# Optimization experiments

Measured on AMD Instinct MI355X. Metric: run time of the kernel, lower is better.

The kernel has to match this reference:

```python
import jax, jax.numpy as jnp
import numpy as np

NUM_NODES = 65536      # 16 graphs x 4096 nodes
NODES_PER_GRAPH = 4096
NUM_GRAPHS = 16
NUM_EDGES = 1048576    # avg degree 16
DIM = 64


def setup_inputs() -> dict:
    key = jax.random.key(0)
    ks = jax.random.split(key, 10)
    # edges constrained within each component graph (batched-graph semantics)
    eper = NUM_EDGES // NUM_GRAPHS
    gid = np.repeat(np.arange(NUM_GRAPHS), eper)
    rng = np.random.default_rng(0)
    src = jnp.asarray(rng.integers(0, NODES_PER_GRAPH, NUM_EDGES) + gid * NODES_PER_GRAPH, dtype=jnp.int64)
    dst = jnp.asarray(rng.integers(0, NODES_PER_GRAPH, NUM_EDGES) + gid * NODES_PER_GRAPH, dtype=jnp.int64)
    s = 1.0 / np.sqrt(DIM)
    return {
        "x": jax.random.normal(ks[0], (NUM_NODES, DIM), dtype=jnp.float32),
        "W1": jax.random.normal(ks[1], (DIM, DIM), dtype=jnp.float32) * s,
        "b1": jnp.zeros((DIM,), dtype=jnp.float32),
        "W2": jax.random.normal(ks[2], (DIM, DIM), dtype=jnp.float32) * s,
        "b2": jnp.zeros((DIM,), dtype=jnp.float32),
        "W3": jax.random.normal(ks[3], (DIM, DIM), dtype=jnp.float32) * s,
        "b3": jnp.zeros((DIM,), dtype=jnp.float32),
        "src": src,
        "dst": dst,
        "num_graphs": NUM_GRAPHS,
    }


def _sym_norms(src, dst, n):
    ones = jnp.ones(src.shape[0], dtype=jnp.float32)
    deg_out = jax.ops.segment_sum(ones, src, num_segments=n)
    deg_in = jax.ops.segment_sum(ones, dst, num_segments=n)
    inv_sqrt = lambda d: jnp.where(d > 0, d, 1.0) ** -0.5 * (d > 0)
    return inv_sqrt(deg_out), inv_sqrt(deg_in)


def _graph_conv(x, W, b, src, dst, norm_src, norm_dst, n):
    # DGL GraphConv, norm='both': h = D_in^{-1/2} A D_out^{-1/2} (X W) + b
    h = (x * norm_src[:, None]) @ W          # [N, D]
    msg = h[src]                              # [E, D] gather
    agg = jax.ops.segment_sum(msg, dst, num_segments=n)  # [N, D] scatter-add
    return agg * norm_dst[:, None] + b


def reference(x, W1, b1, W2, b2, W3, b3, src, dst, num_graphs):
    n = x.shape[0]
    norm_src, norm_dst = _sym_norms(src, dst, n)
    h = _graph_conv(x, W1, b1, src, dst, norm_src, norm_dst, n)
    h = _graph_conv(h, W2, b2, src, dst, norm_src, norm_dst, n)
    h = _graph_conv(h, W3, b3, src, dst, norm_src, norm_dst, n)
    # unbatch + pad to max_num_nodes + stack; equal-size graphs -> pure reshape
    return h.reshape(num_graphs, n // num_graphs, h.shape[-1])
```

## Files before the change

### kernel.cpp

```cpp
#include <hip/hip_runtime.h>
#include <hip/hip_fp16.h>

#define DIM 64
#define NG  16
#define CPG 16
#define NPG 4096
#define LSTR 68
#define HISTB (NG*CPG)
#define GGN 32

__global__ __launch_bounds__(256) void k1_hist_gemm(
    const int* __restrict__ src, const int* __restrict__ dst,
    int* __restrict__ hsub, int* __restrict__ dsub, int chunk, int npg,
    const float* __restrict__ x, const float* __restrict__ W1,
    float* __restrict__ hout, int swiz)
{
    __shared__ int smem[8192];
    const int tid = threadIdx.x;
    if ((int)blockIdx.x < HISTB) {
        int* hs = smem;
        int* hd = smem + NPG;
        const int blk = blockIdx.x;
        const int g = blk / CPG;
        const int ebase = blk * chunk;
        const int nbase = g * npg;
        for (int i = tid; i < npg; i += 256) { hs[i] = 0; hd[i] = 0; }
        __syncthreads();
        for (int e = tid; e < chunk; e += 256) {
            atomicAdd(&hs[src[ebase + e] - nbase], 1);
            atomicAdd(&hd[dst[ebase + e] - nbase], 1);
        }
        __syncthreads();
        for (int i = tid; i < npg; i += 256) {
            hsub[blk * npg + i] = hs[i];
            dsub[blk * npg + i] = hd[i];
        }
    } else {
        float* Wt = (float*)smem;
        float* xs = Wt + 64 * LSTR;
        int blk = blockIdx.x - HISTB;
        if (swiz) {
            int xg = blk & 7;
            int j = blk >> 3;
            int g = xg + ((j >> 7) << 3);
            blk = (g << 7) + (j & 127);
        }
        const int row0 = blk * 32;
        for (int i = tid; i < 64 * 64; i += 256) {
            int k = i >> 6, c = i & 63;
            Wt[c * LSTR + k] = W1[i];
        }
        for (int i = tid; i < 32 * 64; i += 256) {
            int r = i >> 6, c = i & 63;
            xs[r * LSTR + c] = x[(size_t)(row0 + r) * 64 + c];
        }
        __syncthreads();
        const int c0 = tid & 31;
        const int r0 = tid >> 5;
        float acc[4][2] = {};
#pragma unroll
        for (int k = 0; k < 64; k += 4) {
            float4 w0 = *(const float4*)&Wt[(c0     ) * LSTR + k];
            float4 w1 = *(const float4*)&Wt[(c0 + 32) * LSTR + k];
#pragma unroll
            for (int rr = 0; rr < 4; ++rr) {
                float4 xv = *(const float4*)&xs[(r0 + 8 * rr) * LSTR + k];
                acc[rr][0] += xv.x * w0.x + xv.y * w0.y + xv.z * w0.z + xv.w * w0.w;
                acc[rr][1] += xv.x * w1.x + xv.y * w1.y + xv.z * w1.z + xv.w * w1.w;
            }
        }
#pragma unroll
        for (int rr = 0; rr < 4; ++rr) {
            int row = row0 + r0 + 8 * rr;
            hout[(size_t)row * 64 + c0     ] = acc[rr][0];
            hout[(size_t)row * 64 + c0 + 32] = acc[rr][1];
        }
    }
}

__global__ __launch_bounds__(1024) void k2_scan(
    const int* __restrict__ hsub, int* __restrict__ dsub,
    float* __restrict__ ns, float* __restrict__ nd,
    int* __restrict__ rowptr, int epg, int npg, int N, int E)
{
    __shared__ int ddeg[NPG];
    __shared__ int wsum[16];
    const int g = blockIdx.x;
    const int t = threadIdx.x;
    const int nbase = g * npg;
    const int ebase = g * epg;
    for (int i = t; i < npg; i += 1024) {
        int sd = 0, dd = 0;
#pragma unroll
        for (int k = 0; k < CPG; ++k) {
            sd += hsub[(g * CPG + k) * npg + i];
            dd += dsub[(g * CPG + k) * npg + i];
        }
        ns[nbase + i] = sd > 0 ? rsqrtf((float)sd) : 0.0f;
        nd[nbase + i] = dd > 0 ? rsqrtf((float)dd) : 0.0f;
        ddeg[i] = dd;
    }
    __syncthreads();
    const int i0 = 4 * t;
    int d0 = ddeg[i0], d1 = ddeg[i0 + 1], d2 = ddeg[i0 + 2], d3 = ddeg[i0 + 3];
    int s4 = d0 + d1 + d2 + d3;
    const int lane = t & 63, wid = t >> 6;
    int v = s4;
#pragma unroll
    for (int off = 1; off < 64; off <<= 1) {
        int u = __shfl_up(v, off, 64);
        if (lane >= off) v += u;
    }
    if (lane == 63) wsum[wid] = v;
    __syncthreads();
    if (t < 16) {
        int w = wsum[t];
#pragma unroll
        for (int off = 1; off < 16; off <<= 1) {
            int u = __shfl_up(w, off, 16);
            if (t >= off) w += u;
        }
        wsum[t] = w;
    }
    __syncthreads();
    int incl = v + (wid > 0 ? wsum[wid - 1] : 0);
    int c = ebase + incl - s4;
    rowptr[nbase + i0    ] = c; ddeg[i0    ] = c; c += d0;
    rowptr[nbase + i0 + 1] = c; ddeg[i0 + 1] = c; c += d1;
    rowptr[nbase + i0 + 2] = c; ddeg[i0 + 2] = c; c += d2;
    rowptr[nbase + i0 + 3] = c; ddeg[i0 + 3] = c;
    if (g == 0 && t == 0) rowptr[N] = E;
    __syncthreads();
    for (int i = t; i < npg; i += 1024) {
        int cc = ddeg[i];
#pragma unroll
        for (int k = 0; k < CPG; ++k) {
            int* p = &dsub[(g * CPG + k) * npg + i];
            int old = *p; *p = cc; cc += old;
        }
    }
}

__global__ __launch_bounds__(256) void k3_fill(
    const int* __restrict__ src, const int* __restrict__ dst,
    const int* __restrict__ dsub, int* __restrict__ ssrc, int chunk, int npg,
    const float* __restrict__ hA32, const float* __restrict__ ns,
    __half* __restrict__ hF)
{
    const int t = threadIdx.x;
    if ((int)blockIdx.x < HISTB) {
        __shared__ int cur[NPG];
        const int blk = blockIdx.x;
        const int g = blk / CPG;
        const int ebase = blk * chunk;
        const int nbase = g * npg;
        for (int i = t; i < npg; i += 256) cur[i] = dsub[blk * npg + i];
        __syncthreads();
        for (int e = t; e < chunk; e += 256) {
            int s = src[ebase + e];
            int d = dst[ebase + e] - nbase;
            int pos = atomicAdd(&cur[d], 1);
            ssrc[pos] = s;
        }
    } else {
        const int sb = blockIdx.x - HISTB;
        const int base = sb * 16384;
#pragma unroll
        for (int it = 0; it < 16; ++it) {
            int pos = base + it * 1024 + t * 4;
            float4 v = *(const float4*)(hA32 + pos);
            float s = ns[pos >> 6];
            __half2 p0 = __floats2half2_rn(v.x * s, v.y * s);
            __half2 p1 = __floats2half2_rn(v.z * s, v.w * s);
            uint2 o;
            o.x = *(const unsigned int*)&p0;
            o.y = *(const unsigned int*)&p1;
            *(uint2*)(hF + pos) = o;
        }
    }
}

__device__ __forceinline__ void acc_h4(float4& acc, uint2 u)
{
    __half2 p = *(__half2*)&u.x;
    __half2 q = *(__half2*)&u.y;
    float2 f0 = __half22float2(p);
    float2 f1 = __half22float2(q);
    acc.x += f0.x; acc.y += f0.y; acc.z += f1.x; acc.w += f1.y;
}

__device__ __forceinline__ void acc_h4s(float4& acc, uint2 u, float s)
{
    __half2 p = *(__half2*)&u.x;
    __half2 q = *(__half2*)&u.y;
    float2 f0 = __half22float2(p);
    float2 f1 = __half22float2(q);
    acc.x += s * f0.x; acc.y += s * f0.y; acc.z += s * f1.x; acc.w += s * f1.y;
}

__device__ __forceinline__ float4 gather_node(
    const __half* __restrict__ h, const int* __restrict__ ssrc,
    int beg, int end, int sub)
{
    const size_t off = (size_t)sub * 4;
    float4 acc = {0.f, 0.f, 0.f, 0.f};
    int j = beg;
    const int last = end - 8;
    if (j <= last) {
        int s0 = ssrc[j+0], s1 = ssrc[j+1], s2 = ssrc[j+2], s3 = ssrc[j+3];
        int s4 = ssrc[j+4], s5 = ssrc[j+5], s6 = ssrc[j+6], s7 = ssrc[j+7];
        uint2 a0 = *(const uint2*)(h + (size_t)s0 * 64 + off);
        uint2 a1 = *(const uint2*)(h + (size_t)s1 * 64 + off);
        uint2 a2 = *(const uint2*)(h + (size_t)s2 * 64 + off);
        uint2 a3 = *(const uint2*)(h + (size_t)s3 * 64 + off);
        uint2 a4 = *(const uint2*)(h + (size_t)s4 * 64 + off);
        uint2 a5 = *(const uint2*)(h + (size_t)s5 * 64 + off);
        uint2 a6 = *(const uint2*)(h + (size_t)s6 * 64 + off);
        uint2 a7 = *(const uint2*)(h + (size_t)s7 * 64 + off);
        j += 8;
        bool more = (j <= last);
        if (more) {
            s0 = ssrc[j+0]; s1 = ssrc[j+1]; s2 = ssrc[j+2]; s3 = ssrc[j+3];
            s4 = ssrc[j+4]; s5 = ssrc[j+5]; s6 = ssrc[j+6]; s7 = ssrc[j+7];
        }
        while (more) {
            uint2 b0 = *(const uint2*)(h + (size_t)s0 * 64 + off);
            uint2 b1 = *(const uint2*)(h + (size_t)s1 * 64 + off);
            uint2 b2 = *(const uint2*)(h + (size_t)s2 * 64 + off);
            uint2 b3 = *(const uint2*)(h + (size_t)s3 * 64 + off);
            uint2 b4 = *(const uint2*)(h + (size_t)s4 * 64 + off);
            uint2 b5 = *(const uint2*)(h + (size_t)s5 * 64 + off);
            uint2 b6 = *(const uint2*)(h + (size_t)s6 * 64 + off);
            uint2 b7 = *(const uint2*)(h + (size_t)s7 * 64 + off);
            j += 8;
            more = (j <= last);
            if (more) {
                s0 = ssrc[j+0]; s1 = ssrc[j+1]; s2 = ssrc[j+2]; s3 = ssrc[j+3];
                s4 = ssrc[j+4]; s5 = ssrc[j+5]; s6 = ssrc[j+6]; s7 = ssrc[j+7];
            }
            acc_h4(acc, a0); acc_h4(acc, a1); acc_h4(acc, a2); acc_h4(acc, a3);
            acc_h4(acc, a4); acc_h4(acc, a5); acc_h4(acc, a6); acc_h4(acc, a7);
            a0 = b0; a1 = b1; a2 = b2; a3 = b3;
            a4 = b4; a5 = b5; a6 = b6; a7 = b7;
        }
        acc_h4(acc, a0); acc_h4(acc, a1); acc_h4(acc, a2); acc_h4(acc, a3);
        acc_h4(acc, a4); acc_h4(acc, a5); acc_h4(acc, a6); acc_h4(acc, a7);
    }
    int rem = end - j;
    if (rem > 0) {
#pragma unroll
        for (int q = 0; q < 4; ++q) {
            int jj = j + (q < rem ? q : rem - 1);
            int s = ssrc[jj];
            uint2 u = *(const uint2*)(h + (size_t)s * 64 + off);
            acc_h4s(acc, u, (q < rem) ? 1.0f : 0.0f);
        }
        if (rem > 4) {
#pragma unroll
            for (int q = 4; q < 8; ++q) {
                int jj = j + (q < rem ? q : rem - 1);
                int s = ssrc[jj];
                uint2 u = *(const uint2*)(h + (size_t)s * 64 + off);
                acc_h4s(acc, u, (q < rem) ? 1.0f : 0.0f);
            }
        }
    }
    return acc;
}

__global__ __launch_bounds__(256) void gg_kernel(
    const __half* __restrict__ h, const int* __restrict__ ssrc,
    const int* __restrict__ rowptr, const float* __restrict__ ns,
    const float* __restrict__ nd, const float* __restrict__ bprev,
    const float* __restrict__ W, __half* __restrict__ hout,
    int N, int swiz)
{
    __shared__ float Ws[64 * 64];
    __shared__ float us[GGN][64];
    int blk = blockIdx.x;
    if (swiz) {
        int xg = blk & 7;
        int j = blk >> 3;
        int g = xg + ((j >> 7) << 3);
        blk = (g << 7) + (j & 127);
    }
    const int tid = threadIdx.x;
    for (int i = tid; i < 64 * 64; i += 256) Ws[i] = W[i];

    const int wv = tid >> 6;
    const int lane = tid & 63;
    const int grp = lane >> 4;
    const int sub = lane & 15;

#pragma unroll
    for (int p = 0; p < GGN / 16; ++p) {
        int nl = p * 16 + wv * 4 + grp;
        int w = blk * GGN + nl;
        if (w < N) {
            int beg = rowptr[w], end = rowptr[w + 1];
            float4 acc = gather_node(h, ssrc, beg, end, sub);
            float sw = ns[w];
            float alpha = nd[w] * sw;
            float4 bv = *(const float4*)(bprev + sub * 4);
            float4 uo;
            uo.x = acc.x * alpha + sw * bv.x;
            uo.y = acc.y * alpha + sw * bv.y;
            uo.z = acc.z * alpha + sw * bv.z;
            uo.w = acc.w * alpha + sw * bv.w;
            *(float4*)&us[nl][sub * 4] = uo;
        }
    }
    __syncthreads();
    const int c = tid & 63;
#pragma unroll
    for (int m = 0; m < 8; ++m) {
        int nl = (tid >> 6) + 4 * m;
        int w = blk * GGN + nl;
        if (w >= N) continue;
        const float* ur = us[nl];
        float y = 0.f;
#pragma unroll
        for (int k = 0; k < 64; k += 4) {
            float4 uv = *(const float4*)&ur[k];
            y += uv.x * Ws[(k    ) * 64 + c]
               + uv.y * Ws[(k + 1) * 64 + c]
               + uv.z * Ws[(k + 2) * 64 + c]
               + uv.w * Ws[(k + 3) * 64 + c];
        }
        hout[(size_t)w * 64 + c] = __float2half_rn(y);
    }
}

__global__ __launch_bounds__(256) void gather_kernel(
    const __half* __restrict__ h, const int* __restrict__ ssrc,
    const int* __restrict__ rowptr, float* __restrict__ out,
    const float* __restrict__ nd, const float* __restrict__ b,
    int N, int swiz)
{
    int blk = blockIdx.x;
    if (swiz) {
        int x = blk & 7;
        int j = blk >> 3;
        int g = x + ((j >> 8) << 3);
        blk = (g << 8) + (j & 255);
    }
    const int wv = threadIdx.x >> 6;
    const int lane = threadIdx.x & 63;
    const int grp = lane >> 4;
    const int sub = lane & 15;
    int w = blk * 16 + wv * 4 + grp;
    if (w >= N) return;
    int beg = rowptr[w], end = rowptr[w + 1];
    float4 acc = gather_node(h, ssrc, beg, end, sub);
    float n = nd[w];
    const float4 bv = *(const float4*)(b + sub * 4);
    acc.x = acc.x * n + bv.x;
    acc.y = acc.y * n + bv.y;
    acc.z = acc.z * n + bv.z;
    acc.w = acc.w * n + bv.w;
    *(float4*)(out + (size_t)w * 64 + sub * 4) = acc;
}

extern "C" void kernel_launch(void* const* d_in, const int* in_sizes, int n_in,
                              void* d_out, int out_size, void* d_ws, size_t ws_size,
                              hipStream_t stream)
{
    const float* x  = (const float*)d_in[0];
    const float* W1 = (const float*)d_in[1];
    const float* b1 = (const float*)d_in[2];
    const float* W2 = (const float*)d_in[3];
    const float* b2 = (const float*)d_in[4];
    const float* W3 = (const float*)d_in[5];
    const float* b3 = (const float*)d_in[6];
    const int*  src = (const int*)d_in[7];
    const int*  dst = (const int*)d_in[8];

    const int E = in_sizes[7];
    const int N = in_sizes[0] / DIM;
    const int epg = E / NG;
    const int npg = N / NG;
    const int chunk = epg / CPG;

    float*  ns     = (float*)d_ws;
    float*  nd     = ns + N;
    float*  hA32   = nd + N;
    __half* hF     = (__half*)(hA32 + (size_t)N * DIM);
    __half* h2     = hF + (size_t)N * DIM;
    int*    rowptr = (int*)(h2 + (size_t)N * DIM);
    int*    ssrc   = rowptr + N + 1;
    int*    hsub   = ssrc + E;
    int*    dsub   = hsub + (size_t)HISTB * npg;
    float*  agg    = (float*)d_out;

    const int swiz = (N == 65536 && npg == 4096) ? 1 : 0;

    k1_hist_gemm<<<HISTB + N / 32, 256, 0, stream>>>(
        src, dst, hsub, dsub, chunk, npg, x, W1, hA32, swiz);
    k2_scan<<<NG, 1024, 0, stream>>>(
        hsub, dsub, ns, nd, rowptr, epg, npg, N, E);
    k3_fill<<<HISTB + N / 256, 256, 0, stream>>>(
        src, dst, dsub, ssrc, chunk, npg, hA32, ns, hF);

    gg_kernel<<<N / GGN, 256, 0, stream>>>(
        hF, ssrc, rowptr, ns, nd, b1, W2, h2, N, swiz);
    gg_kernel<<<N / GGN, 256, 0, stream>>>(
        h2, ssrc, rowptr, ns, nd, b2, W3, hF, N, swiz);
    gather_kernel<<<N / 16, 256, 0, stream>>>(
        hF, ssrc, rowptr, agg, nd, b3, N, swiz);
}
```

Measured before the change: 231.1 us.

## Gather two nodes per lane group concurrently and read W from global

The gather loop now walks two destination nodes' edge lists in lockstep, issuing 16 independent loads per iteration for more memory-level parallelism, in place of the software-pipelined single-node loop. gg_kernel drops the shared-memory W tile and reads W straight from global/L1, keeping 8 register accumulators per thread so each W element is loaded once per k. The final gather kernel handles 32 nodes per block with half the blocks, and its swizzle is adjusted to match. Bounds checks on N are removed, which assumes N is a multiple of 32, and the imbalance between paired nodes' degrees can leave lanes idle.

```diff
diff --git a/kernel.cpp b/kernel.cpp
--- a/kernel.cpp
+++ b/kernel.cpp
@@ -198,53 +198,26 @@
     acc.x += s * f0.x; acc.y += s * f0.y; acc.z += s * f1.x; acc.w += s * f1.y;
 }
 
-__device__ __forceinline__ float4 gather_node(
+__device__ __forceinline__ void gather_rest(
     const __half* __restrict__ h, const int* __restrict__ ssrc,
-    int beg, int end, int sub)
+    int j, int end, int sub, float4& acc)
 {
     const size_t off = (size_t)sub * 4;
-    float4 acc = {0.f, 0.f, 0.f, 0.f};
-    int j = beg;
     const int last = end - 8;
-    if (j <= last) {
+    while (j <= last) {
         int s0 = ssrc[j+0], s1 = ssrc[j+1], s2 = ssrc[j+2], s3 = ssrc[j+3];
         int s4 = ssrc[j+4], s5 = ssrc[j+5], s6 = ssrc[j+6], s7 = ssrc[j+7];
-        uint2 a0 = *(const uint2*)(h + (size_t)s0 * 64 + off);
-        uint2 a1 = *(const uint2*)(h + (size_t)s1 * 64 + off);
-        uint2 a2 = *(const uint2*)(h + (size_t)s2 * 64 + off);
-        uint2 a3 = *(const uint2*)(h + (size_t)s3 * 64 + off);
-        uint2 a4 = *(const uint2*)(h + (size_t)s4 * 64 + off);
-        uint2 a5 = *(const uint2*)(h + (size_t)s5 * 64 + off);
-        uint2 a6 = *(const uint2*)(h + (size_t)s6 * 64 + off);
-        uint2 a7 = *(const uint2*)(h + (size_t)s7 * 64 + off);
+        uint2 u0 = *(const uint2*)(h + (size_t)s0 * 64 + off);
+        uint2 u1 = *(const uint2*)(h + (size_t)s1 * 64 + off);
+        uint2 u2 = *(const uint2*)(h + (size_t)s2 * 64 + off);
+        uint2 u3 = *(const uint2*)(h + (size_t)s3 * 64 + off);
+        uint2 u4 = *(const uint2*)(h + (size_t)s4 * 64 + off);
+        uint2 u5 = *(const uint2*)(h + (size_t)s5 * 64 + off);
+        uint2 u6 = *(const uint2*)(h + (size_t)s6 * 64 + off);
+        uint2 u7 = *(const uint2*)(h + (size_t)s7 * 64 + off);
+        acc_h4(acc, u0); acc_h4(acc, u1); acc_h4(acc, u2); acc_h4(acc, u3);
+        acc_h4(acc, u4); acc_h4(acc, u5); acc_h4(acc, u6); acc_h4(acc, u7);
         j += 8;
-        bool more = (j <= last);
-        if (more) {
-            s0 = ssrc[j+0]; s1 = ssrc[j+1]; s2 = ssrc[j+2]; s3 = ssrc[j+3];
-            s4 = ssrc[j+4]; s5 = ssrc[j+5]; s6 = ssrc[j+6]; s7 = ssrc[j+7];
-        }
-        while (more) {
-            uint2 b0 = *(const uint2*)(h + (size_t)s0 * 64 + off);
-            uint2 b1 = *(const uint2*)(h + (size_t)s1 * 64 + off);
-            uint2 b2 = *(const uint2*)(h + (size_t)s2 * 64 + off);
-            uint2 b3 = *(const uint2*)(h + (size_t)s3 * 64 + off);
-            uint2 b4 = *(const uint2*)(h + (size_t)s4 * 64 + off);
-            uint2 b5 = *(const uint2*)(h + (size_t)s5 * 64 + off);
-            uint2 b6 = *(const uint2*)(h + (size_t)s6 * 64 + off);
-            uint2 b7 = *(const uint2*)(h + (size_t)s7 * 64 + off);
-            j += 8;
-            more = (j <= last);
-            if (more) {
-                s0 = ssrc[j+0]; s1 = ssrc[j+1]; s2 = ssrc[j+2]; s3 = ssrc[j+3];
-                s4 = ssrc[j+4]; s5 = ssrc[j+5]; s6 = ssrc[j+6]; s7 = ssrc[j+7];
-            }
-            acc_h4(acc, a0); acc_h4(acc, a1); acc_h4(acc, a2); acc_h4(acc, a3);
-            acc_h4(acc, a4); acc_h4(acc, a5); acc_h4(acc, a6); acc_h4(acc, a7);
-            a0 = b0; a1 = b1; a2 = b2; a3 = b3;
-            a4 = b4; a5 = b5; a6 = b6; a7 = b7;
-        }
-        acc_h4(acc, a0); acc_h4(acc, a1); acc_h4(acc, a2); acc_h4(acc, a3);
-        acc_h4(acc, a4); acc_h4(acc, a5); acc_h4(acc, a6); acc_h4(acc, a7);
     }
     int rem = end - j;
     if (rem > 0) {
@@ -265,7 +238,45 @@
             }
         }
     }
-    return acc;
+}
+
+__device__ __forceinline__ void gather_node2(
+    const __half* __restrict__ h, const int* __restrict__ ssrc,
+    int begA, int endA, int begB, int endB, int sub,
+    float4& accA, float4& accB)
+{
+    const size_t off = (size_t)sub * 4;
+    int jA = begA, jB = begB;
+    const int lastA = endA - 8, lastB = endB - 8;
+    while (jA <= lastA && jB <= lastB) {
+        int a0 = ssrc[jA+0], a1 = ssrc[jA+1], a2 = ssrc[jA+2], a3 = ssrc[jA+3];
+        int a4 = ssrc[jA+4], a5 = ssrc[jA+5], a6 = ssrc[jA+6], a7 = ssrc[jA+7];
+        int b0 = ssrc[jB+0], b1 = ssrc[jB+1], b2 = ssrc[jB+2], b3 = ssrc[jB+3];
+        int b4 = ssrc[jB+4], b5 = ssrc[jB+5], b6 = ssrc[jB+6], b7 = ssrc[jB+7];
+        uint2 uA0 = *(const uint2*)(h + (size_t)a0 * 64 + off);
+        uint2 uA1 = *(const uint2*)(h + (size_t)a1 * 64 + off);
+        uint2 uA2 = *(const uint2*)(h + (size_t)a2 * 64 + off);
+        uint2 uA3 = *(const uint2*)(h + (size_t)a3 * 64 + off);
+        uint2 uA4 = *(const uint2*)(h + (size_t)a4 * 64 + off);
+        uint2 uA5 = *(const uint2*)(h + (size_t)a5 * 64 + off);
+        uint2 uA6 = *(const uint2*)(h + (size_t)a6 * 64 + off);
+        uint2 uA7 = *(const uint2*)(h + (size_t)a7 * 64 + off);
+        uint2 uB0 = *(const uint2*)(h + (size_t)b0 * 64 + off);
+        uint2 uB1 = *(const uint2*)(h + (size_t)b1 * 64 + off);
+        uint2 uB2 = *(const uint2*)(h + (size_t)b2 * 64 + off);
+        uint2 uB3 = *(const uint2*)(h + (size_t)b3 * 64 + off);
+        uint2 uB4 = *(const uint2*)(h + (size_t)b4 * 64 + off);
+        uint2 uB5 = *(const uint2*)(h + (size_t)b5 * 64 + off);
+        uint2 uB6 = *(const uint2*)(h + (size_t)b6 * 64 + off);
+        uint2 uB7 = *(const uint2*)(h + (size_t)b7 * 64 + off);
+        acc_h4(accA, uA0); acc_h4(accA, uA1); acc_h4(accA, uA2); acc_h4(accA, uA3);
+        acc_h4(accA, uA4); acc_h4(accA, uA5); acc_h4(accA, uA6); acc_h4(accA, uA7);
+        acc_h4(accB, uB0); acc_h4(accB, uB1); acc_h4(accB, uB2); acc_h4(accB, uB3);
+        acc_h4(accB, uB4); acc_h4(accB, uB5); acc_h4(accB, uB6); acc_h4(accB, uB7);
+        jA += 8; jB += 8;
+    }
+    gather_rest(h, ssrc, jA, endA, sub, accA);
+    gather_rest(h, ssrc, jB, endB, sub, accB);
 }
 
 __global__ __launch_bounds__(256) void gg_kernel(
@@ -275,7 +286,6 @@
     const float* __restrict__ W, __half* __restrict__ hout,
     int N, int swiz)
 {
-    __shared__ float Ws[64 * 64];
     __shared__ float us[GGN][64];
     int blk = blockIdx.x;
     if (swiz) {
@@ -285,49 +295,62 @@
         blk = (g << 7) + (j & 127);
     }
     const int tid = threadIdx.x;
-    for (int i = tid; i < 64 * 64; i += 256) Ws[i] = W[i];
-
     const int wv = tid >> 6;
     const int lane = tid & 63;
     const int grp = lane >> 4;
     const int sub = lane & 15;
 
-#pragma unroll
-    for (int p = 0; p < GGN / 16; ++p) {
-        int nl = p * 16 + wv * 4 + grp;
-        int w = blk * GGN + nl;
-        if (w < N) {
-            int beg = rowptr[w], end = rowptr[w + 1];
-            float4 acc = gather_node(h, ssrc, beg, end, sub);
-            float sw = ns[w];
-            float alpha = nd[w] * sw;
-            float4 bv = *(const float4*)(bprev + sub * 4);
+    const int nlA = wv * 4 + grp;
+    const int nlB = nlA + 16;
+    const int wA = blk * GGN + nlA;
+    const int wB = blk * GGN + nlB;
+    {
+        int begA = rowptr[wA], endA = rowptr[wA + 1];
+        int begB = rowptr[wB], endB = rowptr[wB + 1];
+        float4 accA = {0.f,0.f,0.f,0.f}, accB = {0.f,0.f,0.f,0.f};
+        gather_node2(h, ssrc, begA, endA, begB, endB, sub, accA, accB);
+        float4 bv = *(const float4*)(bprev + sub * 4);
+        {
+            float sw = ns[wA];
+            float alpha = nd[wA] * sw;
             float4 uo;
-            uo.x = acc.x * alpha + sw * bv.x;
-            uo.y = acc.y * alpha + sw * bv.y;
-            uo.z = acc.z * alpha + sw * bv.z;
-            uo.w = acc.w * alpha + sw * bv.w;
-            *(float4*)&us[nl][sub * 4] = uo;
+            uo.x = accA.x * alpha + sw * bv.x;
+            uo.y = accA.y * alpha + sw * bv.y;
+            uo.z = accA.z * alpha + sw * bv.z;
+            uo.w = accA.w * alpha + sw * bv.w;
+            *(float4*)&us[nlA][sub * 4] = uo;
+        }
+        {
+            float sw = ns[wB];
+            float alpha = nd[wB] * sw;
+            float4 uo;
+            uo.x = accB.x * alpha + sw * bv.x;
+            uo.y = accB.y * alpha + sw * bv.y;
+            uo.z = accB.z * alpha + sw * bv.z;
+            uo.w = accB.w * alpha + sw * bv.w;
+            *(float4*)&us[nlB][sub * 4] = uo;
         }
     }
     __syncthreads();
     const int c = tid & 63;
+    const int nb = tid >> 6;
+    float y[8] = {0.f,0.f,0.f,0.f,0.f,0.f,0.f,0.f};
+#pragma unroll
+    for (int k = 0; k < 64; k += 4) {
+        float w0 = W[(k    ) * 64 + c];
+        float w1 = W[(k + 1) * 64 + c];
+        float w2 = W[(k + 2) * 64 + c];
+        float w3 = W[(k + 3) * 64 + c];
+#pragma unroll
+        for (int m = 0; m < 8; ++m) {
+            const float4 uv = *(const float4*)&us[nb + 4 * m][k];
+            y[m] += uv.x * w0 + uv.y * w1 + uv.z * w2 + uv.w * w3;
+        }
+    }
 #pragma unroll
     for (int m = 0; m < 8; ++m) {
-        int nl = (tid >> 6) + 4 * m;
-        int w = blk * GGN + nl;
-        if (w >= N) continue;
-        const float* ur = us[nl];
-        float y = 0.f;
-#pragma unroll
-        for (int k = 0; k < 64; k += 4) {
-            float4 uv = *(const float4*)&ur[k];
-            y += uv.x * Ws[(k    ) * 64 + c]
-               + uv.y * Ws[(k + 1) * 64 + c]
-               + uv.z * Ws[(k + 2) * 64 + c]
-               + uv.w * Ws[(k + 3) * 64 + c];
-        }
-        hout[(size_t)w * 64 + c] = __float2half_rn(y);
+        int wo = blk * GGN + nb + 4 * m;
+        hout[(size_t)wo * 64 + c] = __float2half_rn(y[m]);
     }
 }
 
@@ -341,24 +364,36 @@
     if (swiz) {
         int x = blk & 7;
         int j = blk >> 3;
-        int g = x + ((j >> 8) << 3);
-        blk = (g << 8) + (j & 255);
+        int g = x + ((j >> 7) << 3);
+        blk = (g << 7) + (j & 127);
     }
     const int wv = threadIdx.x >> 6;
     const int lane = threadIdx.x & 63;
     const int grp = lane >> 4;
     const int sub = lane & 15;
-    int w = blk * 16 + wv * 4 + grp;
-    if (w >= N) return;
-    int beg = rowptr[w], end = rowptr[w + 1];
-    float4 acc = gather_node(h, ssrc, beg, end, sub);
-    float n = nd[w];
+    int wA = blk * 32 + wv * 4 + grp;
+    int wB = wA + 16;
+    int begA = rowptr[wA], endA = rowptr[wA + 1];
+    int begB = rowptr[wB], endB = rowptr[wB + 1];
+    float4 accA = {0.f,0.f,0.f,0.f}, accB = {0.f,0.f,0.f,0.f};
+    gather_node2(h, ssrc, begA, endA, begB, endB, sub, accA, accB);
     const float4 bv = *(const float4*)(b + sub * 4);
-    acc.x = acc.x * n + bv.x;
-    acc.y = acc.y * n + bv.y;
-    acc.z = acc.z * n + bv.z;
-    acc.w = acc.w * n + bv.w;
-    *(float4*)(out + (size_t)w * 64 + sub * 4) = acc;
+    {
+        float n = nd[wA];
+        accA.x = accA.x * n + bv.x;
+        accA.y = accA.y * n + bv.y;
+        accA.z = accA.z * n + bv.z;
+        accA.w = accA.w * n + bv.w;
+        *(float4*)(out + (size_t)wA * 64 + sub * 4) = accA;
+    }
+    {
+        float n = nd[wB];
+        accB.x = accB.x * n + bv.x;
+        accB.y = accB.y * n + bv.y;
+        accB.z = accB.z * n + bv.z;
+        accB.w = accB.w * n + bv.w;
+        *(float4*)(out + (size_t)wB * 64 + sub * 4) = accB;
+    }
 }
 
 extern "C" void kernel_launch(void* const* d_in, const int* in_sizes, int n_in,
@@ -405,6 +440,6 @@
         hF, ssrc, rowptr, ns, nd, b1, W2, h2, N, swiz);
     gg_kernel<<<N / GGN, 256, 0, stream>>>(
         h2, ssrc, rowptr, ns, nd, b2, W3, hF, N, swiz);
-    gather_kernel<<<N / 16, 256, 0, stream>>>(
+    gather_kernel<<<N / 32, 256, 0, stream>>>(
         hF, ssrc, rowptr, agg, nd, b3, N, swiz);
 }
```

Result: faster. 218.7 us (-5.4%).
